# Kernel optimization log

Measured on AMD Instinct MI355X. Metric: run time of the kernel, lower is better.

Reference implementation:

```python
import jax, jax.numpy as jnp
import numpy as np

B, T, C, H = 256, 256, 1024, 64

def setup_inputs() -> dict:
    key = jax.random.key(0)
    kx, kk, kq, kv = jax.random.split(key, 4)
    x = jax.random.normal(kx, (B, T, C), dtype=jnp.float32)
    # Dense kernels init'd with normal(stddev=0.02), stored as [in, out] like flax
    Wk = jax.random.normal(kk, (C, H), dtype=jnp.float32) * 0.02
    Wq = jax.random.normal(kq, (C, H), dtype=jnp.float32) * 0.02
    Wv = jax.random.normal(kv, (C, H), dtype=jnp.float32) * 0.02
    return {"x": x, "Wk": Wk, "Wq": Wq, "Wv": Wv}

def reference(x, Wk, Wq, Wv):
    # single-head causal self-attention (eval mode: dropout is identity)
    k = jnp.einsum('btc,ch->bth', x, Wk)      # [B,T,H]
    q = jnp.einsum('btc,ch->bth', x, Wq)      # [B,T,H]
    v = jnp.einsum('btc,ch->bth', x, Wv)      # [B,T,H]
    scale = jnp.asarray(k.shape[-1], k.dtype) ** -0.5
    wei = jnp.einsum('bth,bsh->bts', q, k) * scale  # [B,T,T]
    t = x.shape[1]
    causal = jnp.tril(jnp.ones((t, t), dtype=bool))
    wei = jnp.where(causal, wei, -jnp.inf)
    wei = jax.nn.softmax(wei, axis=-1)
    out = jnp.einsum('bts,bsh->bth', wei, v)  # [B,T,H]
    return out
```

## Files before the change

kernel.cpp:

```cpp
#include <hip/hip_runtime.h>
#include <hip/hip_bf16.h>

typedef float f32x4 __attribute__((ext_vector_type(4)));
typedef short s16x8 __attribute__((ext_vector_type(8)));

__device__ __forceinline__ unsigned short f2bf(float f) {
    union { float f; unsigned u; } v; v.f = f;
    unsigned r = v.u + 0x7FFF + ((v.u >> 16) & 1);
    return (unsigned short)(r >> 16);
}

__global__ void prep_w(const float* __restrict__ Wk, const float* __restrict__ Wq,
                       const float* __restrict__ Wv, unsigned short* __restrict__ wt) {
    int n = blockIdx.x;
    int tid = threadIdx.x;
    const float* src; int col; float sc = 1.0f;
    if (n < 64)       { src = Wq; col = n;       sc = 0.125f; }
    else if (n < 128) { src = Wk; col = n - 64; }
    else              { src = Wv; col = n - 128; }
#pragma unroll
    for (int i = 0; i < 4; i++) {
        int c = i * 256 + tid;
        wt[n * 1024 + c] = f2bf(src[c * 64 + col] * sc);
    }
}

__global__ __launch_bounds__(256) void proj_kernel(const float* __restrict__ x,
                                                   const unsigned short* __restrict__ wt,
                                                   unsigned short* __restrict__ qkv) {
    __shared__ unsigned short xs[128 * 72];

    const int tid  = threadIdx.x;
    const int lane = tid & 63;
    const int wid  = tid >> 6;
    const int quad = lane >> 4;
    const int l15  = lane & 15;
    const int wm   = wid >> 1;
    const int wn   = wid & 1;
    const long blockM = (long)blockIdx.x * 128;

    f32x4 acc[4][6] = {};

    const int srow = tid >> 4;
    const int scol = tid & 15;
    const float* xbase = x + (blockM + srow) * 1024 + scol * 4;

    for (int k0 = 0; k0 < 1024; k0 += 64) {
        __syncthreads();
#pragma unroll
        for (int p = 0; p < 8; p++) {
            const float4 v = *(const float4*)(xbase + (long)p * 16 * 1024 + k0);
            ushort4 bv;
            bv.x = f2bf(v.x); bv.y = f2bf(v.y); bv.z = f2bf(v.z); bv.w = f2bf(v.w);
            *(ushort4*)&xs[(srow + p * 16) * 72 + scol * 4] = bv;
        }
        __syncthreads();
#pragma unroll
        for (int kk = 0; kk < 64; kk += 32) {
            s16x8 a[4], bf[6];
#pragma unroll
            for (int mt = 0; mt < 4; mt++)
                a[mt] = *(const s16x8*)&xs[(wm * 64 + mt * 16 + l15) * 72 + kk + quad * 8];
#pragma unroll
            for (int nt = 0; nt < 6; nt++)
                bf[nt] = *(const s16x8*)&wt[(long)(wn * 96 + nt * 16 + l15) * 1024 + k0 + kk + quad * 8];
#pragma unroll
            for (int mt = 0; mt < 4; mt++)
#pragma unroll
                for (int nt = 0; nt < 6; nt++)
                    acc[mt][nt] = __builtin_amdgcn_mfma_f32_16x16x32_bf16(a[mt], bf[nt], acc[mt][nt], 0, 0, 0);
        }
    }

#pragma unroll
    for (int mt = 0; mt < 4; mt++)
#pragma unroll
        for (int nt = 0; nt < 6; nt++)
#pragma unroll
            for (int r = 0; r < 4; r++) {
                long row = blockM + wm * 64 + mt * 16 + quad * 4 + r;
                int  col = wn * 96 + nt * 16 + l15;
                qkv[row * 192 + col] = f2bf(acc[mt][nt][r]);
            }
}

__global__ __launch_bounds__(256) void attn_kernel(const unsigned short* __restrict__ qkv,
                                                   float* __restrict__ out) {
    __shared__ unsigned short Vt[64 * 264];
    __shared__ unsigned short Pl[4][16 * 56];

    const int tid  = threadIdx.x;
    const int lane = tid & 63;
    const int wid  = tid >> 6;
    const int quad = lane >> 4;
    const int l15  = lane & 15;
    const int b    = blockIdx.x >> 1;
    const int half = blockIdx.x & 1;

    const unsigned short* qb = qkv + (long)b * 256 * 192;

    {
        const int vs = tid >> 2;
        const int vh = (tid & 3) * 16;
        const int npass = half ? 4 : 2;
        for (int p = 0; p < npass; p++) {
            int s = p * 64 + vs;
            const unsigned short* src = qb + s * 192 + 128 + vh;
            s16x8 v0 = *(const s16x8*)src;
            s16x8 v1 = *(const s16x8*)(src + 8);
#pragma unroll
            for (int i = 0; i < 8; i++) Vt[(vh + i) * 264 + s]     = (unsigned short)v0[i];
#pragma unroll
            for (int i = 0; i < 8; i++) Vt[(vh + 8 + i) * 264 + s] = (unsigned short)v1[i];
        }
    }
    __syncthreads();

    const int base = half * 128 + wid * 32;

    s16x8 qf[2][2];
#pragma unroll
    for (int mt = 0; mt < 2; mt++)
#pragma unroll
        for (int ks = 0; ks < 2; ks++)
            qf[mt][ks] = *(const s16x8*)(qb + (long)(base + mt * 16 + l15) * 192 + ks * 32 + quad * 8);

    f32x4 o[2][4] = {};
    float mr[2][4], lr[2][4];
#pragma unroll
    for (int mt = 0; mt < 2; mt++)
#pragma unroll
        for (int r = 0; r < 4; r++) { mr[mt][r] = -1e30f; lr[mt][r] = 0.0f; }

    const int nst = base / 32 + 1;
    for (int st = 0; st < nst; st++) {
        const int s0 = st * 32;
        s16x8 kf[2][2], vf[4];
#pragma unroll
        for (int sub = 0; sub < 2; sub++)
#pragma unroll
            for (int ks = 0; ks < 2; ks++)
                kf[sub][ks] = *(const s16x8*)(qb + (long)(s0 + sub * 16 + l15) * 192 + 64 + ks * 32 + quad * 8);
#pragma unroll
        for (int n = 0; n < 4; n++)
            vf[n] = *(const s16x8*)&Vt[(n * 16 + l15) * 264 + s0 + quad * 8];

#pragma unroll
        for (int mt = 0; mt < 2; mt++) {
            const int tmin = base + mt * 16;
            f32x4 S0 = {0.f, 0.f, 0.f, 0.f}, S1 = {0.f, 0.f, 0.f, 0.f};
            S0 = __builtin_amdgcn_mfma_f32_16x16x32_bf16(qf[mt][0], kf[0][0], S0, 0, 0, 0);
            S0 = __builtin_amdgcn_mfma_f32_16x16x32_bf16(qf[mt][1], kf[0][1], S0, 0, 0, 0);
            S1 = __builtin_amdgcn_mfma_f32_16x16x32_bf16(qf[mt][0], kf[1][0], S1, 0, 0, 0);
            S1 = __builtin_amdgcn_mfma_f32_16x16x32_bf16(qf[mt][1], kf[1][1], S1, 0, 0, 0);

            if (s0 + 31 > tmin) {
#pragma unroll
                for (int r = 0; r < 4; r++) {
                    int t = tmin + quad * 4 + r;
                    if (s0 + l15 > t)      S0[r] = -1e30f;
                    if (s0 + 16 + l15 > t) S1[r] = -1e30f;
                }
            }

            float a4[4];
#pragma unroll
            for (int r = 0; r < 4; r++) {
                float rm = fmaxf(S0[r], S1[r]);
                rm = fmaxf(rm, __shfl_xor(rm, 1));
                rm = fmaxf(rm, __shfl_xor(rm, 2));
                rm = fmaxf(rm, __shfl_xor(rm, 4));
                rm = fmaxf(rm, __shfl_xor(rm, 8));
                float mn = fmaxf(mr[mt][r], rm);
                float al = exp2f((mr[mt][r] - mn) * 1.44269504f);
                mr[mt][r] = mn;
                float p0 = exp2f((S0[r] - mn) * 1.44269504f);
                float p1 = exp2f((S1[r] - mn) * 1.44269504f);
                float rs = p0 + p1;
                rs += __shfl_xor(rs, 1);
                rs += __shfl_xor(rs, 2);
                rs += __shfl_xor(rs, 4);
                rs += __shfl_xor(rs, 8);
                lr[mt][r] = al * lr[mt][r] + rs;
                a4[r] = al;
                Pl[wid][(quad * 4 + r) * 56 + l15]      = f2bf(p0);
                Pl[wid][(quad * 4 + r) * 56 + l15 + 16] = f2bf(p1);
            }
#pragma unroll
            for (int n = 0; n < 4; n++) {
                f32x4 t = o[mt][n];
#pragma unroll
                for (int r = 0; r < 4; r++) t[r] *= a4[r];
                o[mt][n] = t;
            }
            s16x8 pf = *(const s16x8*)&Pl[wid][l15 * 56 + quad * 8];
#pragma unroll
            for (int n = 0; n < 4; n++)
                o[mt][n] = __builtin_amdgcn_mfma_f32_16x16x32_bf16(pf, vf[n], o[mt][n], 0, 0, 0);
        }
    }

#pragma unroll
    for (int mt = 0; mt < 2; mt++) {
        float inv[4];
#pragma unroll
        for (int r = 0; r < 4; r++) inv[r] = 1.0f / lr[mt][r];
#pragma unroll
        for (int n = 0; n < 4; n++)
#pragma unroll
            for (int r = 0; r < 4; r++) {
                long t = (long)b * 256 + base + mt * 16 + quad * 4 + r;
                out[t * 64 + n * 16 + l15] = o[mt][n][r] * inv[r];
            }
    }
}

extern "C" void kernel_launch(void* const* d_in, const int* in_sizes, int n_in,
                              void* d_out, int out_size, void* d_ws, size_t ws_size,
                              hipStream_t stream) {
    const float* x  = (const float*)d_in[0];
    const float* Wk = (const float*)d_in[1];
    const float* Wq = (const float*)d_in[2];
    const float* Wv = (const float*)d_in[3];
    float* out = (float*)d_out;

    unsigned short* wt  = (unsigned short*)d_ws;
    unsigned short* qkv = wt + 192 * 1024;

    prep_w<<<192, 256, 0, stream>>>(Wk, Wq, Wv, wt);
    proj_kernel<<<512, 256, 0, stream>>>(x, wt, qkv);
    attn_kernel<<<512, 256, 0, stream>>>(qkv, out);
}
```

Baseline: 426.5 us.

## Load x fragments directly from global into registers, dropping LDS staging in projection

The projection kernel no longer stages x tiles through shared memory with barriers. Each wave now loads its MFMA A fragments straight from global fp32, converts them to bf16 with a packed perm-based conversion, and runs the MFMAs, with launch bounds raised to two blocks per CU. The bf16 conversion also changes from round-to-nearest-even to a simpler round-half-up. This removes LDS traffic and syncs, but x rows are read by both wn waves, so global/L2 reads double and the access pattern (strided per-lane 32B chunks) is less coalesced.

Result: slower. 458.4 us (+7.5%).

```diff
diff --git a/kernel.cpp b/kernel.cpp
--- a/kernel.cpp
+++ b/kernel.cpp
@@ -5,9 +5,13 @@
 typedef short s16x8 __attribute__((ext_vector_type(8)));
 
 __device__ __forceinline__ unsigned short f2bf(float f) {
-    union { float f; unsigned u; } v; v.f = f;
-    unsigned r = v.u + 0x7FFF + ((v.u >> 16) & 1);
-    return (unsigned short)(r >> 16);
+    return (unsigned short)((__float_as_uint(f) + 0x8000u) >> 16);
+}
+
+__device__ __forceinline__ unsigned pk2bf(float lo, float hi) {
+    unsigned a = __float_as_uint(lo) + 0x8000u;
+    unsigned b = __float_as_uint(hi) + 0x8000u;
+    return __builtin_amdgcn_perm(b, a, 0x07060302u);
 }
 
 __global__ void prep_w(const float* __restrict__ Wk, const float* __restrict__ Wq,
@@ -25,11 +29,9 @@
     }
 }
 
-__global__ __launch_bounds__(256) void proj_kernel(const float* __restrict__ x,
-                                                   const unsigned short* __restrict__ wt,
-                                                   unsigned short* __restrict__ qkv) {
-    __shared__ unsigned short xs[128 * 72];
-
+__global__ __launch_bounds__(256, 2) void proj_kernel(const float* __restrict__ x,
+                                                      const unsigned short* __restrict__ wt,
+                                                      unsigned short* __restrict__ qkv) {
     const int tid  = threadIdx.x;
     const int lane = tid & 63;
     const int wid  = tid >> 6;
@@ -39,37 +41,42 @@
     const int wn   = wid & 1;
     const long blockM = (long)blockIdx.x * 128;
 
+    const float* ab[4];
+#pragma unroll
+    for (int mt = 0; mt < 4; mt++)
+        ab[mt] = x + (blockM + wm * 64 + mt * 16 + l15) * 1024 + quad * 8;
+    const unsigned short* bb[6];
+#pragma unroll
+    for (int nt = 0; nt < 6; nt++)
+        bb[nt] = wt + (long)(wn * 96 + nt * 16 + l15) * 1024 + quad * 8;
+
     f32x4 acc[4][6] = {};
 
-    const int srow = tid >> 4;
-    const int scol = tid & 15;
-    const float* xbase = x + (blockM + srow) * 1024 + scol * 4;
-
-    for (int k0 = 0; k0 < 1024; k0 += 64) {
-        __syncthreads();
-#pragma unroll
-        for (int p = 0; p < 8; p++) {
-            const float4 v = *(const float4*)(xbase + (long)p * 16 * 1024 + k0);
-            ushort4 bv;
-            bv.x = f2bf(v.x); bv.y = f2bf(v.y); bv.z = f2bf(v.z); bv.w = f2bf(v.w);
-            *(ushort4*)&xs[(srow + p * 16) * 72 + scol * 4] = bv;
+#pragma unroll 2
+    for (int k0 = 0; k0 < 1024; k0 += 32) {
+        s16x8 bfrag[6];
+#pragma unroll
+        for (int nt = 0; nt < 6; nt++)
+            bfrag[nt] = *(const s16x8*)(bb[nt] + k0);
+
+        s16x8 afrag[4];
+#pragma unroll
+        for (int mt = 0; mt < 4; mt++) {
+            const f32x4 lo = *(const f32x4*)(ab[mt] + k0);
+            const f32x4 hi = *(const f32x4*)(ab[mt] + k0 + 4);
+            union { unsigned u[4]; s16x8 v; } pk;
+            pk.u[0] = pk2bf(lo[0], lo[1]);
+            pk.u[1] = pk2bf(lo[2], lo[3]);
+            pk.u[2] = pk2bf(hi[0], hi[1]);
+            pk.u[3] = pk2bf(hi[2], hi[3]);
+            afrag[mt] = pk.v;
         }
-        __syncthreads();
-#pragma unroll
-        for (int kk = 0; kk < 64; kk += 32) {
-            s16x8 a[4], bf[6];
-#pragma unroll
-            for (int mt = 0; mt < 4; mt++)
-                a[mt] = *(const s16x8*)&xs[(wm * 64 + mt * 16 + l15) * 72 + kk + quad * 8];
+
+#pragma unroll
+        for (int mt = 0; mt < 4; mt++)
 #pragma unroll
             for (int nt = 0; nt < 6; nt++)
-                bf[nt] = *(const s16x8*)&wt[(long)(wn * 96 + nt * 16 + l15) * 1024 + k0 + kk + quad * 8];
-#pragma unroll
-            for (int mt = 0; mt < 4; mt++)
-#pragma unroll
-                for (int nt = 0; nt < 6; nt++)
-                    acc[mt][nt] = __builtin_amdgcn_mfma_f32_16x16x32_bf16(a[mt], bf[nt], acc[mt][nt], 0, 0, 0);
-        }
+                acc[mt][nt] = __builtin_amdgcn_mfma_f32_16x16x32_bf16(afrag[mt], bfrag[nt], acc[mt][nt], 0, 0, 0);
     }
 
 #pragma unroll
```

## Double-buffer x tiles in projection GEMM and cheapen bf16 packing

Applied to the files above, without the earlier changes.

The projection kernel now keeps two LDS buffers for x. While MFMAs run on the current tile, the next tile's fp32 loads are issued into registers, then converted and stored to the other buffer. This removes one barrier per k-step and hides global load latency. The bf16 conversion also changes from round-to-nearest-even to plain round-half-up, with two values packed per 32-bit word through a perm instruction. The price is more register pressure from holding the prefetched tile and slightly different rounding.

Measured after the change: 430.9 us. No clear change (+1.0%).

```diff
diff --git a/kernel.cpp b/kernel.cpp
--- a/kernel.cpp
+++ b/kernel.cpp
@@ -5,9 +5,13 @@
 typedef short s16x8 __attribute__((ext_vector_type(8)));
 
 __device__ __forceinline__ unsigned short f2bf(float f) {
-    union { float f; unsigned u; } v; v.f = f;
-    unsigned r = v.u + 0x7FFF + ((v.u >> 16) & 1);
-    return (unsigned short)(r >> 16);
+    return (unsigned short)((__float_as_uint(f) + 0x8000u) >> 16);
+}
+
+__device__ __forceinline__ unsigned pk2bf(float lo, float hi) {
+    unsigned a = __float_as_uint(lo) + 0x8000u;
+    unsigned b = __float_as_uint(hi) + 0x8000u;
+    return __builtin_amdgcn_perm(b, a, 0x07060302u);
 }
 
 __global__ void prep_w(const float* __restrict__ Wk, const float* __restrict__ Wq,
@@ -28,7 +32,7 @@
 __global__ __launch_bounds__(256) void proj_kernel(const float* __restrict__ x,
                                                    const unsigned short* __restrict__ wt,
                                                    unsigned short* __restrict__ qkv) {
-    __shared__ unsigned short xs[128 * 72];
+    __shared__ unsigned short xs[2 * 128 * 72];
 
     const int tid  = threadIdx.x;
     const int lane = tid & 63;
@@ -39,36 +43,61 @@
     const int wn   = wid & 1;
     const long blockM = (long)blockIdx.x * 128;
 
-    f32x4 acc[4][6] = {};
-
     const int srow = tid >> 4;
     const int scol = tid & 15;
     const float* xbase = x + (blockM + srow) * 1024 + scol * 4;
 
-    for (int k0 = 0; k0 < 1024; k0 += 64) {
+    f32x4 acc[4][6] = {};
+    f32x4 st[8];
+
+#pragma unroll
+    for (int p = 0; p < 8; p++)
+        st[p] = *(const f32x4*)(xbase + (long)p * 16 * 1024);
+#pragma unroll
+    for (int p = 0; p < 8; p++) {
+        uint2 w;
+        w.x = pk2bf(st[p][0], st[p][1]);
+        w.y = pk2bf(st[p][2], st[p][3]);
+        *(uint2*)&xs[(srow + p * 16) * 72 + scol * 4] = w;
+    }
+
+#pragma unroll 2
+    for (int s = 0; s < 16; s++) {
+        const int k0  = s * 64;
+        const int cur = (s & 1) * (128 * 72);
+        const int nxt = ((s & 1) ^ 1) * (128 * 72);
         __syncthreads();
-#pragma unroll
-        for (int p = 0; p < 8; p++) {
-            const float4 v = *(const float4*)(xbase + (long)p * 16 * 1024 + k0);
-            ushort4 bv;
-            bv.x = f2bf(v.x); bv.y = f2bf(v.y); bv.z = f2bf(v.z); bv.w = f2bf(v.w);
-            *(ushort4*)&xs[(srow + p * 16) * 72 + scol * 4] = bv;
-        }
-        __syncthreads();
+
+        if (s < 15) {
+#pragma unroll
+            for (int p = 0; p < 8; p++)
+                st[p] = *(const f32x4*)(xbase + (long)p * 16 * 1024 + k0 + 64);
+        }
+
 #pragma unroll
         for (int kk = 0; kk < 64; kk += 32) {
-            s16x8 a[4], bf[6];
+            s16x8 a[4], bfr[6];
 #pragma unroll
             for (int mt = 0; mt < 4; mt++)
-                a[mt] = *(const s16x8*)&xs[(wm * 64 + mt * 16 + l15) * 72 + kk + quad * 8];
+                a[mt] = *(const s16x8*)&xs[cur + (wm * 64 + mt * 16 + l15) * 72 + kk + quad * 8];
 #pragma unroll
             for (int nt = 0; nt < 6; nt++)
-                bf[nt] = *(const s16x8*)&wt[(long)(wn * 96 + nt * 16 + l15) * 1024 + k0 + kk + quad * 8];
+                bfr[nt] = *(const s16x8*)&wt[(long)(wn * 96 + nt * 16 + l15) * 1024 + k0 + kk + quad * 8];
 #pragma unroll
             for (int mt = 0; mt < 4; mt++)
 #pragma unroll
                 for (int nt = 0; nt < 6; nt++)
-                    acc[mt][nt] = __builtin_amdgcn_mfma_f32_16x16x32_bf16(a[mt], bf[nt], acc[mt][nt], 0, 0, 0);
+                    acc[mt][nt] = __builtin_amdgcn_mfma_f32_16x16x32_bf16(a[mt], bfr[nt], acc[mt][nt], 0, 0, 0);
+        }
+
+        if (s < 15) {
+#pragma unroll
+            for (int p = 0; p < 8; p++) {
+                uint2 w;
+                w.x = pk2bf(st[p][0], st[p][1]);
+                w.y = pk2bf(st[p][2], st[p][3]);
+                *(uint2*)&xs[nxt + (srow + p * 16) * 72 + scol * 4] = w;
+            }
         }
     }
 
```
